# Optimization experiments

Measured on AMD Instinct MI355X. Metric: run time of the kernel, lower is better.

Reference implementation:

```python
import jax, jax.numpy as jnp
import numpy as np

B, N, C, H, REG = 1, 2309, 1024, 16, 5
D = C // H


def setup_inputs() -> dict:
    key = jax.random.key(0)
    k0, k1, k2, k3 = jax.random.split(key, 4)
    x = jax.random.normal(k0, (B, N, C), dtype=jnp.float32)
    g_info = jax.random.normal(k1, (12, 2, C), dtype=jnp.float32)
    W_qkv = jax.random.normal(k2, (C, 3 * C), dtype=jnp.float32) * 0.02
    W_proj = jax.random.normal(k3, (C, C), dtype=jnp.float32) * 0.02
    b_proj = jnp.zeros((C,), dtype=jnp.float32)
    return {"x": x, "g_info": g_info, "W_qkv": W_qkv, "W_proj": W_proj, "b_proj": b_proj}


def reference(x, g_info, W_qkv, W_proj, b_proj):
    Bx, Nx, Cx = x.shape
    scale = D ** -0.5
    # qkv projection (qkv_bias=False)
    qkv = (x @ W_qkv).reshape(Bx, Nx, 3, H, D)
    q, k, v = qkv[:, :, 0], qkv[:, :, 1], qkv[:, :, 2]  # [B,N,H,D]

    # grounding query vector from layer 0
    g_layer = g_info[0].reshape(-1, H, D)
    q_g = g_layer[0]  # [H,D]

    # cosine-similarity routing over non-register tokens
    q_pure = q[:, REG:]  # [B,M,H,D]
    q_n = q_pure / jnp.linalg.norm(q_pure, axis=-1, keepdims=True)
    qg_n = q_g / jnp.linalg.norm(q_g, axis=-1, keepdims=True)
    sim = (qg_n[None, None] * q_n).sum(-1).mean(-1)  # [B,M]
    sim = (sim - sim.min()) / (sim.max() - sim.min())  # global min-max normalize
    pos = sim > 0.9  # [B,M] boolean routing mask

    # Full logits computed once; group attention = masked softmax over the
    # group's key set (registers always included). This is mathematically
    # identical to the torch gather->attend->scatter, with static shapes.
    logits = jnp.einsum('bqhd,bkhd->bhqk', q * scale, k)  # [B,H,N,N]

    def masked_attn(tok_mask):
        key_mask = jnp.concatenate([jnp.ones((Bx, REG), bool), tok_mask], axis=1)  # [B,N]
        l = jnp.where(key_mask[:, None, None, :], logits, -jnp.inf)
        a = jax.nn.softmax(l, axis=-1)
        return jnp.einsum('bhqk,bkhd->bqhd', a, v)  # [B,N,H,D]

    x_pos = masked_attn(pos)
    x_neg = masked_attn(~pos)

    reg_out = (x_pos[:, :REG] + x_neg[:, :REG]) * 0.5
    tok_out = jnp.where(pos[:, :, None, None], x_pos[:, REG:], x_neg[:, REG:])
    out = jnp.concatenate([reg_out, tok_out], axis=1).reshape(Bx, Nx, Cx)
    return out @ W_proj + b_proj
```

## Files before the change

kernel.cpp:

```cpp
#include <hip/hip_runtime.h>
#include <math.h>

#define TOK 2309
#define CH 1024
#define NH 16
#define HD 64
#define NREG 5
#define NTOK (TOK - NREG)
#define NPADQ 2432
#define NPAD2 2432
#define NKT 38
#define HTILES 19
#define NQROW 2368
#define QSCL 0.1803368801f

typedef unsigned short ushort_t;
typedef unsigned char uchar_t;
typedef __attribute__((ext_vector_type(8))) short s8frag;
typedef __attribute__((ext_vector_type(4))) float f4frag;
typedef __attribute__((ext_vector_type(2))) long ll2;

__device__ __forceinline__ unsigned short f2bf(float x){
  union { float f; unsigned u; } v; v.f = x;
  unsigned r = v.u + 0x7FFF + ((v.u >> 16) & 1);
  return (unsigned short)(r >> 16);
}
__device__ __forceinline__ float bf2f(unsigned short u){
  union { unsigned u32; float f; } v; v.u32 = ((unsigned)u) << 16;
  return v.f;
}
__device__ __forceinline__ unsigned pack_bf16(float lo, float hi){
  union { float f; unsigned u; } a, b;
  a.f = lo; b.f = hi;
  return __builtin_amdgcn_perm(b.u + 0x8000u, a.u + 0x8000u, 0x07060302u);
}
__device__ __forceinline__ uchar_t f2fp8(float x){
  return (uchar_t)(__builtin_amdgcn_cvt_pk_fp8_f32(x, x, 0, false) & 0xff);
}
__device__ __forceinline__ void cp16(const void* g, void* l){
  __builtin_amdgcn_global_load_lds(
      (const __attribute__((address_space(1))) unsigned int*)g,
      (__attribute__((address_space(3))) unsigned int*)l, 16, 0, 0);
}

__global__ __launch_bounds__(256) void prep_kernel(
    const float* __restrict__ X, const float* __restrict__ Wqkv,
    const float* __restrict__ Wproj, const float* __restrict__ G,
    ushort_t* __restrict__ Xbf, ushort_t* __restrict__ WqkvT,
    ushort_t* __restrict__ WprojT, float* __restrict__ UT)
{
  const int tid = threadIdx.x;
  int bx = blockIdx.x;
  if (bx < NPADQ) {
    const int row = bx;
    const int c4 = tid * 4;
    ushort4 h4 = {0,0,0,0};
    if (row < TOK) {
      float4 v = *(const float4*)&X[(size_t)row*CH + c4];
      h4.x = f2bf(v.x); h4.y = f2bf(v.y); h4.z = f2bf(v.z); h4.w = f2bf(v.w);
    }
    *(ushort4*)&Xbf[(size_t)row*CH + c4] = h4;
    return;
  }
  bx -= NPADQ;
  if (bx < 1024) {
    __shared__ float T[64][68];
    int nb_i = bx & 63;
    const int k0 = (bx >> 6) * 64;
    const float* W; ushort_t* WT; int N;
    if (nb_i < 48) { W = Wqkv; WT = WqkvT; N = 3*CH; }
    else           { W = Wproj; WT = WprojT; N = CH; nb_i -= 48; }
    const int n0 = nb_i * 64;
    const int lr = tid >> 4;
    const int lc = (tid & 15) * 4;
    #pragma unroll
    for (int s = 0; s < 4; s++) {
      float4 v = *(const float4*)&W[(size_t)(k0 + lr + s*16) * N + n0 + lc];
      *(float4*)&T[lr + s*16][lc] = v;
    }
    __syncthreads();
    const int nl = tid >> 2;
    const int kc = (tid & 3) * 16;
    ushort_t* dh = WT + (size_t)(n0 + nl) * CH + k0 + kc;
    #pragma unroll
    for (int g = 0; g < 4; g++) {
      ushort4 oh;
      oh.x = f2bf(T[kc+g*4+0][nl]); oh.y = f2bf(T[kc+g*4+1][nl]);
      oh.z = f2bf(T[kc+g*4+2][nl]); oh.w = f2bf(T[kc+g*4+3][nl]);
      *(ushort4*)&dh[g*4] = oh;
    }
    return;
  }
  bx -= 1024;
  {
    const int k = bx * 16 + (tid >> 4);
    const int h = tid & 15;
    const float* g = G + h*64;
    float n2 = 0.f;
    #pragma unroll
    for (int d = 0; d < 64; d += 4) {
      float4 gv = *(const float4*)&g[d];
      n2 += gv.x*gv.x + gv.y*gv.y + gv.z*gv.z + gv.w*gv.w;
    }
    const float inv = 1.f / sqrtf(n2);
    const float* wr = Wqkv + (size_t)k*(3*CH) + h*64;
    float dot = 0.f;
    #pragma unroll
    for (int d = 0; d < 64; d += 4) {
      float4 wv = *(const float4*)&wr[d];
      float4 gv = *(const float4*)&g[d];
      dot += wv.x*gv.x + wv.y*gv.y + wv.z*gv.z + wv.w*gv.w;
    }
    UT[k*16 + h] = dot * inv;
  }
}

__global__ __launch_bounds__(256) void gemm_qkv_mfma(
    const ushort_t* __restrict__ Xbf, const ushort_t* __restrict__ WT,
    ushort_t* __restrict__ Qbf, uchar_t* __restrict__ Q8,
    uchar_t* __restrict__ K8, ushort_t* __restrict__ Vbf)
{
  __shared__ ushort_t LA[2][4096];
  __shared__ ushort_t LB[2][4096];
  const int tid = threadIdx.x;
  const int w = tid >> 6, lane = tid & 63;
  const int quad = lane >> 4, c16 = lane & 15;
  const int wm = w >> 1, wn = w & 1;
  const int nt = blockIdx.x, mt = blockIdx.y;
  const int n0 = nt * 128, m0 = mt * 128;

  const int srow = tid >> 2;
  const int g = (tid & 3) ^ ((tid >> 3) & 3);
  const size_t aoff = (size_t)(m0 + srow)*CH + g*8;
  const size_t boff = (size_t)(n0 + srow)*CH + g*8;
  const int lbase = (tid & 192) * 8;

  f4frag acc[4][4];
  #pragma unroll
  for (int mi = 0; mi < 4; mi++)
    #pragma unroll
    for (int nb = 0; nb < 4; nb++) acc[mi][nb] = (f4frag){0.f,0.f,0.f,0.f};

  const int soff = (quad ^ ((c16 >> 1) & 3)) * 8;
  int aro[4], bro[4];
  #pragma unroll
  for (int i = 0; i < 4; i++) {
    aro[i] = (wm*64 + i*16 + c16)*32 + soff;
    bro[i] = (wn*64 + i*16 + c16)*32 + soff;
  }

#define QKV_STAGE(KT, BUF) {                                                   \
    const int _k = (KT)*32;                                                    \
    cp16(Xbf + aoff + _k,                 &LA[BUF][lbase]);                    \
    cp16(Xbf + aoff + _k + (size_t)64*CH, &LA[BUF][2048 + lbase]);             \
    cp16(WT  + boff + _k,                 &LB[BUF][lbase]);                    \
    cp16(WT  + boff + _k + (size_t)64*CH, &LB[BUF][2048 + lbase]);             \
    }

  QKV_STAGE(0, 0);
  for (int kt = 0; kt < 32; kt++) {
    const int buf = kt & 1;
    __syncthreads();
    if (kt < 31) { QKV_STAGE(kt+1, buf^1); }
    s8frag a[4], b[4];
    #pragma unroll
    for (int i = 0; i < 4; i++) a[i] = *(const s8frag*)&LA[buf][aro[i]];
    #pragma unroll
    for (int i = 0; i < 4; i++) b[i] = *(const s8frag*)&LB[buf][bro[i]];
    #pragma unroll
    for (int mi = 0; mi < 4; mi++)
      #pragma unroll
      for (int nb = 0; nb < 4; nb++)
        acc[mi][nb] = __builtin_amdgcn_mfma_f32_16x16x32_bf16(a[mi], b[nb], acc[mi][nb], 0, 0, 0);
  }
#undef QKV_STAGE

  const int three = (nt >= 16) ? 2 : (nt >= 8) ? 1 : 0;
  #pragma unroll
  for (int mi = 0; mi < 4; mi++) {
    const int orow = m0 + wm*64 + mi*16 + quad*4;
    if (three == 0) {
      #pragma unroll
      for (int nb = 0; nb < 4; nb++) {
        const int col = n0 + wn*64 + nb*16 + c16;
        const int h = (col >> 6) & 15, d = col & 63;
        ushort_t* qb = Qbf + (size_t)h*NPADQ*64;
        uchar_t*  q8 = Q8 + (size_t)h*NPADQ*64;
        #pragma unroll
        for (int r = 0; r < 4; r++) {
          int row = orow + r;
          float v = (row < TOK) ? acc[mi][nb][r] : 0.f;
          qb[(size_t)row*64 + d] = f2bf(v);
          q8[(size_t)row*64 + d] = f2fp8(v);
        }
      }
    } else if (three == 1) {
      #pragma unroll
      for (int nb = 0; nb < 4; nb++) {
        const int col = n0 + wn*64 + nb*16 + c16;
        const int h = (col >> 6) & 15;
        const int quadK = ((nb & 1) * 2) + (c16 >> 3);
        const int byteoff = (nb >> 1) * 8 + (c16 & 7);
        uchar_t* base = K8 + (size_t)h*NKT*4096;
        #pragma unroll
        for (int r = 0; r < 4; r++) {
          int row = orow + r;
          float v = (row < TOK) ? acc[mi][nb][r] * QSCL : 0.f;
          int tile = row >> 6, b = (row >> 4) & 3, c16K = row & 15;
          base[(size_t)tile*4096 + b*1024 + (quadK*16 + c16K)*16 + byteoff] = f2fp8(v);
        }
      }
    } else {
      const int tile  = orow >> 6;
      const int jj    = orow & 63;
      const int c     = jj >> 5;
      const int t16   = (jj >> 4) & 1;
      const int quadA = (jj >> 2) & 3;
      #pragma unroll
      for (int nb = 0; nb < 4; nb++) {
        const int col = n0 + wn*64 + nb*16 + c16;
        const int h = (col >> 6) & 15, d = col & 63;
        const int dblk = d >> 4, c16A = d & 15;
        ushort_t* base = Vbf + (size_t)h*NKT*4096;
        ushort4 o;
        o.x = f2bf((orow+0 < TOK) ? acc[mi][nb][0] : 0.f);
        o.y = f2bf((orow+1 < TOK) ? acc[mi][nb][1] : 0.f);
        o.z = f2bf((orow+2 < TOK) ? acc[mi][nb][2] : 0.f);
        o.w = f2bf((orow+3 < TOK) ? acc[mi][nb][3] : 0.f);
        *(ushort4*)&base[(size_t)tile*4096 + dblk*1024 + c*512
                         + (quadA*16 + c16A)*8 + 4*t16] = o;
      }
    }
  }
}

__global__ __launch_bounds__(256) void sim_kernel(
    const float* __restrict__ X, const float* __restrict__ UT,
    const ushort_t* __restrict__ Qbf, float* __restrict__ sim)
{
  __shared__ float xs[1024];
  __shared__ float pnum[16][17];
  __shared__ float pn2[16][17];
  const int tid = threadIdx.x;
  const int row = NREG + blockIdx.x;
  *(float4*)&xs[tid*4] = *(const float4*)&X[(size_t)row*CH + tid*4];
  __syncthreads();
  const int h = tid & 15, seg = tid >> 4;
  const int k0 = seg * 64;
  float num = 0.f;
  #pragma unroll
  for (int j = 0; j < 64; j++)
    num += xs[k0 + j] * UT[(k0 + j)*16 + h];
  const ushort_t* qr = Qbf + ((size_t)h*NPADQ + row)*64 + seg*4;
  ushort4 a = *(const ushort4*)qr;
  float q0 = bf2f(a.x), q1 = bf2f(a.y), q2 = bf2f(a.z), q3 = bf2f(a.w);
  pnum[seg][h] = num;
  pn2[seg][h] = q0*q0 + q1*q1 + q2*q2 + q3*q3;
  __syncthreads();
  if (tid < 16) {
    float nsum = 0.f, dsum = 0.f;
    #pragma unroll
    for (int s = 0; s < 16; s++) { nsum += pnum[s][tid]; dsum += pn2[s][tid]; }
    float acc = nsum / sqrtf(dsum);
    acc += __shfl_xor(acc, 1, 64);
    acc += __shfl_xor(acc, 2, 64);
    acc += __shfl_xor(acc, 4, 64);
    acc += __shfl_xor(acc, 8, 64);
    if (tid == 0) sim[blockIdx.x] = acc * (1.0f/16.0f);
  }
}

__global__ __launch_bounds__(256) void mask_kernel(
    const float* __restrict__ sim, int* __restrict__ cls,
    float* __restrict__ WP, float* __restrict__ WN)
{
  __shared__ float smn[256], smx[256];
  const int tid = threadIdx.x;
  float mn = 1e30f, mx = -1e30f;
  for (int i = tid; i < NTOK; i += 256) { float s = sim[i]; mn = fminf(mn, s); mx = fmaxf(mx, s); }
  smn[tid] = mn; smx[tid] = mx;
  __syncthreads();
  for (int off = 128; off > 0; off >>= 1) {
    if (tid < off) { smn[tid] = fminf(smn[tid], smn[tid+off]); smx[tid] = fmaxf(smx[tid], smx[tid+off]); }
    __syncthreads();
  }
  mn = smn[0]; mx = smx[0];
  float inv = 1.0f / (mx - mn);
  for (int j = tid; j < NPAD2; j += 256) {
    float wp = 0.f, wn = 0.f; int c = 0;
    if (j < NREG) { wp = 1.f; wn = 1.f; c = 2; }
    else if (j < TOK) {
      bool pos = ((sim[j-NREG] - mn) * inv) > 0.9f;
      c = pos ? 1 : 0;
      wp = pos ? 1.f : 0.f;
      wn = pos ? 0.f : 1.f;
    }
    WP[j] = wp; WN[j] = wn;
    if (j < TOK) cls[j] = c;
  }
}

__global__ __launch_bounds__(256) void attn_kernel(
    const uchar_t* __restrict__ Q8, const uchar_t* __restrict__ K8,
    const ushort_t* __restrict__ Vbf,
    const float* __restrict__ WP, const float* __restrict__ WN,
    ushort_t* __restrict__ POp, ushort_t* __restrict__ POn,
    float* __restrict__ Lp, float* __restrict__ Ln)
{
  __shared__ __align__(16) uchar_t smem[24576];
  uchar_t* Kst = smem;
  uchar_t* Vst = smem + 8192;
  const int tid = threadIdx.x;
  const int w = tid >> 6, lane = tid & 63;
  const int quad = lane >> 4, c16 = lane & 15;
  const int h = blockIdx.y;
  const int half = blockIdx.z;
  const int q0 = blockIdx.x * 64;

  const uchar_t* Qh = Q8 + (size_t)h * NPADQ * 64;
  const uchar_t* gk = K8 + ((size_t)h*NKT + half*HTILES)*4096 + tid*16;
  const uchar_t* gv = (const uchar_t*)Vbf + ((size_t)h*NKT + half*HTILES)*8192 + tid*16;
  const int lw = w * 1024;

  const uchar_t* qp = Qh + (size_t)(q0 + w*16 + c16)*64 + quad*8;
  const long qf0 = *(const long*)(qp);
  const long qf1 = *(const long*)(qp + 32);

  f4frag op[4], on[4];
  #pragma unroll
  for (int nb = 0; nb < 4; nb++) { op[nb] = (f4frag){0.f,0.f,0.f,0.f}; on[nb] = (f4frag){0.f,0.f,0.f,0.f}; }
  float lp = 0.f, ln = 0.f;

  cp16(gk, Kst + lw);
  cp16(gv, Vst + lw);
  cp16(gv + 4096, Vst + 4096 + lw);

  int pb = 0;
  for (int t = 0; t < HTILES; t++) {
    __syncthreads();
    if (t < HTILES-1) {
      cp16(gk + (size_t)(t+1)*4096, Kst + (pb^1)*4096 + lw);
      cp16(gv + (size_t)(t+1)*8192,        Vst + (pb^1)*8192 + lw);
      cp16(gv + (size_t)(t+1)*8192 + 4096, Vst + (pb^1)*8192 + 4096 + lw);
    }
    const int j0 = half*(HTILES*64) + t*64;
    f4frag st[4];
    #pragma unroll
    for (int b = 0; b < 4; b++) {
      ll2 kv = *(const ll2*)&Kst[pb*4096 + b*1024 + lane*16];
      f4frag z = (f4frag){0.f,0.f,0.f,0.f};
      z     = __builtin_amdgcn_mfma_f32_16x16x32_fp8_fp8(kv.x, qf0, z, 0, 0, 0);
      st[b] = __builtin_amdgcn_mfma_f32_16x16x32_fp8_fp8(kv.y, qf1, z, 0, 0, 0);
    }
    unsigned pu[4][2], nu[4][2];
    #pragma unroll
    for (int b = 0; b < 4; b++) {
      float4 wp4 = *(const float4*)&WP[j0 + b*16 + quad*4];
      float4 wn4 = *(const float4*)&WN[j0 + b*16 + quad*4];
      float p0 = __builtin_amdgcn_exp2f(st[b][0]);
      float p1 = __builtin_amdgcn_exp2f(st[b][1]);
      float p2 = __builtin_amdgcn_exp2f(st[b][2]);
      float p3 = __builtin_amdgcn_exp2f(st[b][3]);
      float a0 = p0*wp4.x, a1 = p1*wp4.y, a2 = p2*wp4.z, a3 = p3*wp4.w;
      float b0 = p0*wn4.x, b1 = p1*wn4.y, b2 = p2*wn4.z, b3 = p3*wn4.w;
      lp += (a0+a1)+(a2+a3);
      ln += (b0+b1)+(b2+b3);
      pu[b][0] = pack_bf16(a0, a1); pu[b][1] = pack_bf16(a2, a3);
      nu[b][0] = pack_bf16(b0, b1); nu[b][1] = pack_bf16(b2, b3);
    }
    union Frag { unsigned u[4]; s8frag v; };
    Frag fp0, fp1, fn0, fn1;
    fp0.u[0]=pu[0][0]; fp0.u[1]=pu[0][1]; fp0.u[2]=pu[1][0]; fp0.u[3]=pu[1][1];
    fp1.u[0]=pu[2][0]; fp1.u[1]=pu[2][1]; fp1.u[2]=pu[3][0]; fp1.u[3]=pu[3][1];
    fn0.u[0]=nu[0][0]; fn0.u[1]=nu[0][1]; fn0.u[2]=nu[1][0]; fn0.u[3]=nu[1][1];
    fn1.u[0]=nu[2][0]; fn1.u[1]=nu[2][1]; fn1.u[2]=nu[3][0]; fn1.u[3]=nu[3][1];
    #pragma unroll
    for (int nb = 0; nb < 4; nb++) {
      s8frag va = *(const s8frag*)&Vst[pb*8192 + nb*2048 + lane*16];
      s8frag vb = *(const s8frag*)&Vst[pb*8192 + nb*2048 + 1024 + lane*16];
      op[nb] = __builtin_amdgcn_mfma_f32_16x16x32_bf16(va, fp0.v, op[nb], 0, 0, 0);
      op[nb] = __builtin_amdgcn_mfma_f32_16x16x32_bf16(vb, fp1.v, op[nb], 0, 0, 0);
      on[nb] = __builtin_amdgcn_mfma_f32_16x16x32_bf16(va, fn0.v, on[nb], 0, 0, 0);
      on[nb] = __builtin_amdgcn_mfma_f32_16x16x32_bf16(vb, fn1.v, on[nb], 0, 0, 0);
    }
    pb ^= 1;
  }

  lp += __shfl_xor(lp, 16, 64); lp += __shfl_xor(lp, 32, 64);
  ln += __shfl_xor(ln, 16, 64); ln += __shfl_xor(ln, 32, 64);
  const int iq = q0 + w*16 + c16;
  if (quad == 0 && iq < TOK) {
    Lp[((size_t)half*NH + h)*NQROW + iq] = lp;
    Ln[((size_t)half*NH + h)*NQROW + iq] = ln;
  }
  if (iq < TOK) {
    const size_t base = (size_t)half*NQROW*CH + (size_t)iq*CH + h*HD;
    #pragma unroll
    for (int nb = 0; nb < 4; nb++) {
      uint2 po, no;
      po.x = pack_bf16(op[nb][0], op[nb][1]);
      po.y = pack_bf16(op[nb][2], op[nb][3]);
      no.x = pack_bf16(on[nb][0], on[nb][1]);
      no.y = pack_bf16(on[nb][2], on[nb][3]);
      *(uint2*)(POp + base + nb*16 + quad*4) = po;
      *(uint2*)(POn + base + nb*16 + quad*4) = no;
    }
  }
}

__global__ __launch_bounds__(256) void merge_kernel(
    const ushort_t* __restrict__ POp, const ushort_t* __restrict__ POn,
    const float* __restrict__ Lp, const float* __restrict__ Ln,
    const int* __restrict__ cls, ushort_t* __restrict__ AObf)
{
  const int row = blockIdx.x;
  const int c4 = threadIdx.x * 4;
  const int h = c4 >> 6;
  const size_t o0 = (size_t)row*CH + c4;
  const size_t o1 = (size_t)NQROW*CH + o0;
  ushort4 p0 = *(const ushort4*)(POp + o0);
  ushort4 p1 = *(const ushort4*)(POp + o1);
  ushort4 n0 = *(const ushort4*)(POn + o0);
  ushort4 n1 = *(const ushort4*)(POn + o1);
  const float lpt = Lp[(size_t)h*NQROW + row] + Lp[(size_t)(NH+h)*NQROW + row];
  const float lnt = Ln[(size_t)h*NQROW + row] + Ln[(size_t)(NH+h)*NQROW + row];
  const float ilp = 1.f / lpt, iln = 1.f / lnt;
  const int cq = cls[row];
  float vp[4], vn[4], o[4];
  vp[0] = (bf2f(p0.x)+bf2f(p1.x))*ilp; vn[0] = (bf2f(n0.x)+bf2f(n1.x))*iln;
  vp[1] = (bf2f(p0.y)+bf2f(p1.y))*ilp; vn[1] = (bf2f(n0.y)+bf2f(n1.y))*iln;
  vp[2] = (bf2f(p0.z)+bf2f(p1.z))*ilp; vn[2] = (bf2f(n0.z)+bf2f(n1.z))*iln;
  vp[3] = (bf2f(p0.w)+bf2f(p1.w))*ilp; vn[3] = (bf2f(n0.w)+bf2f(n1.w))*iln;
  if (row < NREG) {
    #pragma unroll
    for (int i = 0; i < 4; i++) o[i] = 0.5f*(vp[i]+vn[i]);
  } else if (cq == 1) {
    #pragma unroll
    for (int i = 0; i < 4; i++) o[i] = vp[i];
  } else {
    #pragma unroll
    for (int i = 0; i < 4; i++) o[i] = vn[i];
  }
  uint2 pk;
  pk.x = pack_bf16(o[0], o[1]);
  pk.y = pack_bf16(o[2], o[3]);
  *(uint2*)(AObf + (size_t)row*CH + c4) = pk;
}

__global__ __launch_bounds__(256) void gemm_proj_mfma(
    const ushort_t* __restrict__ A, const ushort_t* __restrict__ WT,
    const float* __restrict__ bp, float* __restrict__ out)
{
  __shared__ ushort_t LA[2][4096];
  __shared__ ushort_t LB[2][2048];
  const int tid = threadIdx.x;
  const int w = tid >> 6, lane = tid & 63;
  const int quad = lane >> 4, c16 = lane & 15;
  const int wm = w >> 1, wn = w & 1;
  const int nt = blockIdx.x, mt = blockIdx.y;
  const int n0 = nt * 64, m0 = mt * 128;

  const int srow = tid >> 2;
  const int g = (tid & 3) ^ ((tid >> 3) & 3);
  const size_t aoff = (size_t)(m0 + srow)*CH + g*8;
  const size_t boff = (size_t)(n0 + srow)*CH + g*8;
  const int lbase = (tid & 192) * 8;

  f4frag acc[4][2];
  #pragma unroll
  for (int mi = 0; mi < 4; mi++)
    #pragma unroll
    for (int nb = 0; nb < 2; nb++) acc[mi][nb] = (f4frag){0.f,0.f,0.f,0.f};

  const int soff = (quad ^ ((c16 >> 1) & 3)) * 8;
  int aro[4], bro[2];
  #pragma unroll
  for (int i = 0; i < 4; i++) aro[i] = (wm*64 + i*16 + c16)*32 + soff;
  #pragma unroll
  for (int i = 0; i < 2; i++) bro[i] = (wn*32 + i*16 + c16)*32 + soff;

#define PROJ_STAGE(KT, BUF) {                                                  \
    const int _k = (KT)*32;                                                    \
    cp16(A  + aoff + _k,                 &LA[BUF][lbase]);                     \
    cp16(A  + aoff + _k + (size_t)64*CH, &LA[BUF][2048 + lbase]);              \
    cp16(WT + boff + _k,                 &LB[BUF][lbase]);                     \
    }

  PROJ_STAGE(0, 0);
  for (int kt = 0; kt < 32; kt++) {
    const int buf = kt & 1;
    __syncthreads();
    if (kt < 31) { PROJ_STAGE(kt+1, buf^1); }
    s8frag a[4], b[2];
    #pragma unroll
    for (int i = 0; i < 4; i++) a[i] = *(const s8frag*)&LA[buf][aro[i]];
    #pragma unroll
    for (int i = 0; i < 2; i++) b[i] = *(const s8frag*)&LB[buf][bro[i]];
    #pragma unroll
    for (int mi = 0; mi < 4; mi++)
      #pragma unroll
      for (int nb = 0; nb < 2; nb++)
        acc[mi][nb] = __builtin_amdgcn_mfma_f32_16x16x32_bf16(a[mi], b[nb], acc[mi][nb], 0, 0, 0);
  }
#undef PROJ_STAGE

  #pragma unroll
  for (int mi = 0; mi < 4; mi++) {
    const int orow = m0 + wm*64 + mi*16 + quad*4;
    #pragma unroll
    for (int nb = 0; nb < 2; nb++) {
      const int col = n0 + wn*32 + nb*16 + c16;
      const float bias = bp[col];
      #pragma unroll
      for (int r = 0; r < 4; r++) {
        int row = orow + r;
        if (row < TOK) out[(size_t)row*CH + col] = acc[mi][nb][r] + bias;
      }
    }
  }
}

extern "C" void kernel_launch(void* const* d_in, const int* in_sizes, int n_in,
                              void* d_out, int out_size, void* d_ws, size_t ws_size,
                              hipStream_t stream) {
  const float* x      = (const float*)d_in[0];
  const float* g_info = (const float*)d_in[1];
  const float* W_qkv  = (const float*)d_in[2];
  const float* W_proj = (const float*)d_in[3];
  const float* b_proj = (const float*)d_in[4];
  float* out = (float*)d_out;

  float* ws = (float*)d_ws;
  float* SIM = ws;
  float* WP  = SIM + NTOK;
  float* WN  = WP + NPAD2;
  int*   CLS = (int*)(WN + NPAD2);
  float* LpB = (float*)(CLS + 2312);
  float* LnB = LpB + (size_t)2*NH*NQROW;
  float* UT  = LnB + (size_t)2*NH*NQROW;
  ushort_t* Xbf    = (ushort_t*)(UT + (size_t)CH*NH);
  ushort_t* WqkvT  = Xbf    + (size_t)NPADQ*CH;
  ushort_t* WprojT = WqkvT  + (size_t)3*CH*CH;
  ushort_t* Qbf    = WprojT + (size_t)CH*CH;
  ushort_t* AObf   = Qbf    + (size_t)NH*NPADQ*64;
  ushort_t* POp    = AObf   + (size_t)NPADQ*CH;
  ushort_t* POn    = POp    + (size_t)2*NQROW*CH;
  uchar_t*  Q8     = (uchar_t*)(POn + (size_t)2*NQROW*CH);
  uchar_t*  K8     = Q8 + (size_t)NH*NPADQ*64;
  ushort_t* Vbf    = (ushort_t*)(K8 + (size_t)NH*NKT*4096);

  prep_kernel<<<dim3(NPADQ + 1024 + 64), 256, 0, stream>>>(
      x, W_qkv, W_proj, g_info, Xbf, WqkvT, WprojT, UT);
  gemm_qkv_mfma<<<dim3(24, 19), 256, 0, stream>>>(Xbf, WqkvT, Qbf, Q8, K8, Vbf);
  sim_kernel<<<dim3(NTOK), 256, 0, stream>>>(x, UT, Qbf, SIM);
  mask_kernel<<<dim3(1), 256, 0, stream>>>(SIM, CLS, WP, WN);
  attn_kernel<<<dim3(37, NH, 2), 256, 0, stream>>>(Q8, K8, Vbf, WP, WN,
                                                   POp, POn, LpB, LnB);
  merge_kernel<<<dim3(TOK), 256, 0, stream>>>(POp, POn, LpB, LnB, CLS, AObf);
  gemm_proj_mfma<<<dim3(16, 19), 256, 0, stream>>>(AObf, WprojT, b_proj, out);
}
```

Before: 232.2 us.

## Compute only each query's own group attention, dual path for registers only

Each non-register query row now computes only the masked attention for its own group (selected per lane via the class array), instead of both positive and negative groups. Only the first query block, which holds the register tokens, still computes both and writes fp32 partials to a small side buffer. This halves the PV MFMAs, exp masking work and partial-output traffic, and simplifies the merge kernel. The per-lane selection of the weight row and the divergent branch on the first block add small overhead.

Measured after the change: 240.2 us. 3.5% more time.

```diff
diff --git a/kernel.cpp b/kernel.cpp
--- a/kernel.cpp
+++ b/kernel.cpp
@@ -271,8 +271,7 @@
 }
 
 __global__ __launch_bounds__(256) void mask_kernel(
-    const float* __restrict__ sim, int* __restrict__ cls,
-    float* __restrict__ WP, float* __restrict__ WN)
+    const float* __restrict__ sim, int* __restrict__ cls, float* __restrict__ WSL)
 {
   __shared__ float smn[256], smx[256];
   const int tid = threadIdx.x;
@@ -295,7 +294,8 @@
       wp = pos ? 1.f : 0.f;
       wn = pos ? 0.f : 1.f;
     }
-    WP[j] = wp; WN[j] = wn;
+    WSL[j] = wn;
+    WSL[NPAD2 + j] = wp;
     if (j < TOK) cls[j] = c;
   }
 }
@@ -303,9 +303,10 @@
 __global__ __launch_bounds__(256) void attn_kernel(
     const uchar_t* __restrict__ Q8, const uchar_t* __restrict__ K8,
     const ushort_t* __restrict__ Vbf,
-    const float* __restrict__ WP, const float* __restrict__ WN,
-    ushort_t* __restrict__ POp, ushort_t* __restrict__ POn,
-    float* __restrict__ Lp, float* __restrict__ Ln)
+    const float* __restrict__ WSL, const int* __restrict__ cls,
+    ushort_t* __restrict__ POs, float* __restrict__ Ls,
+    float* __restrict__ Rp, float* __restrict__ Rn,
+    float* __restrict__ RLp, float* __restrict__ RLn)
 {
   __shared__ __align__(16) uchar_t smem[24576];
   uchar_t* Kst = smem;
@@ -316,6 +317,13 @@
   const int h = blockIdx.y;
   const int half = blockIdx.z;
   const int q0 = blockIdx.x * 64;
+  const bool dual = (blockIdx.x == 0);
+
+  const int iq = q0 + w*16 + c16;
+  const int cq = (iq < TOK) ? cls[iq] : 0;
+  const int sel = (cq != 0) ? 1 : 0;
+  const float* wsel = WSL + (size_t)sel*NPAD2;
+  const float* woth = WSL + (size_t)(1-sel)*NPAD2;
 
   const uchar_t* Qh = Q8 + (size_t)h * NPADQ * 64;
   const uchar_t* gk = K8 + ((size_t)h*NKT + half*HTILES)*4096 + tid*16;
@@ -335,6 +343,7 @@
   cp16(gv, Vst + lw);
   cp16(gv + 4096, Vst + 4096 + lw);
 
+  union Frag { unsigned u[4]; s8frag v; };
   int pb = 0;
   for (int t = 0; t < HTILES; t++) {
     __syncthreads();
@@ -355,91 +364,101 @@
     unsigned pu[4][2], nu[4][2];
     #pragma unroll
     for (int b = 0; b < 4; b++) {
-      float4 wp4 = *(const float4*)&WP[j0 + b*16 + quad*4];
-      float4 wn4 = *(const float4*)&WN[j0 + b*16 + quad*4];
+      float4 w4 = *(const float4*)&wsel[j0 + b*16 + quad*4];
       float p0 = __builtin_amdgcn_exp2f(st[b][0]);
       float p1 = __builtin_amdgcn_exp2f(st[b][1]);
       float p2 = __builtin_amdgcn_exp2f(st[b][2]);
       float p3 = __builtin_amdgcn_exp2f(st[b][3]);
-      float a0 = p0*wp4.x, a1 = p1*wp4.y, a2 = p2*wp4.z, a3 = p3*wp4.w;
-      float b0 = p0*wn4.x, b1 = p1*wn4.y, b2 = p2*wn4.z, b3 = p3*wn4.w;
+      float a0 = p0*w4.x, a1 = p1*w4.y, a2 = p2*w4.z, a3 = p3*w4.w;
       lp += (a0+a1)+(a2+a3);
-      ln += (b0+b1)+(b2+b3);
       pu[b][0] = pack_bf16(a0, a1); pu[b][1] = pack_bf16(a2, a3);
-      nu[b][0] = pack_bf16(b0, b1); nu[b][1] = pack_bf16(b2, b3);
-    }
-    union Frag { unsigned u[4]; s8frag v; };
-    Frag fp0, fp1, fn0, fn1;
+      if (dual) {
+        float4 wo = *(const float4*)&woth[j0 + b*16 + quad*4];
+        float b0 = p0*wo.x, b1 = p1*wo.y, b2 = p2*wo.z, b3 = p3*wo.w;
+        ln += (b0+b1)+(b2+b3);
+        nu[b][0] = pack_bf16(b0, b1); nu[b][1] = pack_bf16(b2, b3);
+      }
+    }
+    Frag fp0, fp1;
     fp0.u[0]=pu[0][0]; fp0.u[1]=pu[0][1]; fp0.u[2]=pu[1][0]; fp0.u[3]=pu[1][1];
     fp1.u[0]=pu[2][0]; fp1.u[1]=pu[2][1]; fp1.u[2]=pu[3][0]; fp1.u[3]=pu[3][1];
-    fn0.u[0]=nu[0][0]; fn0.u[1]=nu[0][1]; fn0.u[2]=nu[1][0]; fn0.u[3]=nu[1][1];
-    fn1.u[0]=nu[2][0]; fn1.u[1]=nu[2][1]; fn1.u[2]=nu[3][0]; fn1.u[3]=nu[3][1];
+    Frag fn0, fn1;
+    if (dual) {
+      fn0.u[0]=nu[0][0]; fn0.u[1]=nu[0][1]; fn0.u[2]=nu[1][0]; fn0.u[3]=nu[1][1];
+      fn1.u[0]=nu[2][0]; fn1.u[1]=nu[2][1]; fn1.u[2]=nu[3][0]; fn1.u[3]=nu[3][1];
+    }
     #pragma unroll
     for (int nb = 0; nb < 4; nb++) {
       s8frag va = *(const s8frag*)&Vst[pb*8192 + nb*2048 + lane*16];
       s8frag vb = *(const s8frag*)&Vst[pb*8192 + nb*2048 + 1024 + lane*16];
       op[nb] = __builtin_amdgcn_mfma_f32_16x16x32_bf16(va, fp0.v, op[nb], 0, 0, 0);
       op[nb] = __builtin_amdgcn_mfma_f32_16x16x32_bf16(vb, fp1.v, op[nb], 0, 0, 0);
-      on[nb] = __builtin_amdgcn_mfma_f32_16x16x32_bf16(va, fn0.v, on[nb], 0, 0, 0);
-      on[nb] = __builtin_amdgcn_mfma_f32_16x16x32_bf16(vb, fn1.v, on[nb], 0, 0, 0);
+      if (dual) {
+        on[nb] = __builtin_amdgcn_mfma_f32_16x16x32_bf16(va, fn0.v, on[nb], 0, 0, 0);
+        on[nb] = __builtin_amdgcn_mfma_f32_16x16x32_bf16(vb, fn1.v, on[nb], 0, 0, 0);
+      }
     }
     pb ^= 1;
   }
 
   lp += __shfl_xor(lp, 16, 64); lp += __shfl_xor(lp, 32, 64);
-  ln += __shfl_xor(ln, 16, 64); ln += __shfl_xor(ln, 32, 64);
-  const int iq = q0 + w*16 + c16;
-  if (quad == 0 && iq < TOK) {
-    Lp[((size_t)half*NH + h)*NQROW + iq] = lp;
-    Ln[((size_t)half*NH + h)*NQROW + iq] = ln;
-  }
+  if (quad == 0 && iq < TOK) Ls[((size_t)half*NH + h)*NQROW + iq] = lp;
   if (iq < TOK) {
     const size_t base = (size_t)half*NQROW*CH + (size_t)iq*CH + h*HD;
     #pragma unroll
     for (int nb = 0; nb < 4; nb++) {
-      uint2 po, no;
+      uint2 po;
       po.x = pack_bf16(op[nb][0], op[nb][1]);
       po.y = pack_bf16(op[nb][2], op[nb][3]);
-      no.x = pack_bf16(on[nb][0], on[nb][1]);
-      no.y = pack_bf16(on[nb][2], on[nb][3]);
-      *(uint2*)(POp + base + nb*16 + quad*4) = po;
-      *(uint2*)(POn + base + nb*16 + quad*4) = no;
+      *(uint2*)(POs + base + nb*16 + quad*4) = po;
+    }
+  }
+  if (dual && w == 0 && c16 < NREG) {
+    ln += __shfl_xor(ln, 16, 64); ln += __shfl_xor(ln, 32, 64);
+    float* rp = Rp + (((size_t)half*NH + h)*NREG + c16)*64;
+    float* rn = Rn + (((size_t)half*NH + h)*NREG + c16)*64;
+    #pragma unroll
+    for (int nb = 0; nb < 4; nb++) {
+      *(f4frag*)&rp[nb*16 + quad*4] = op[nb];
+      *(f4frag*)&rn[nb*16 + quad*4] = on[nb];
+    }
+    if (quad == 0) {
+      RLp[((size_t)half*NH + h)*NREG + c16] = lp;
+      RLn[((size_t)half*NH + h)*NREG + c16] = ln;
     }
   }
 }
 
 __global__ __launch_bounds__(256) void merge_kernel(
-    const ushort_t* __restrict__ POp, const ushort_t* __restrict__ POn,
-    const float* __restrict__ Lp, const float* __restrict__ Ln,
-    const int* __restrict__ cls, ushort_t* __restrict__ AObf)
+    const ushort_t* __restrict__ POs, const float* __restrict__ Ls,
+    const float* __restrict__ Rp, const float* __restrict__ Rn,
+    const float* __restrict__ RLp, const float* __restrict__ RLn,
+    ushort_t* __restrict__ AObf)
 {
   const int row = blockIdx.x;
   const int c4 = threadIdx.x * 4;
   const int h = c4 >> 6;
-  const size_t o0 = (size_t)row*CH + c4;
-  const size_t o1 = (size_t)NQROW*CH + o0;
-  ushort4 p0 = *(const ushort4*)(POp + o0);
-  ushort4 p1 = *(const ushort4*)(POp + o1);
-  ushort4 n0 = *(const ushort4*)(POn + o0);
-  ushort4 n1 = *(const ushort4*)(POn + o1);
-  const float lpt = Lp[(size_t)h*NQROW + row] + Lp[(size_t)(NH+h)*NQROW + row];
-  const float lnt = Ln[(size_t)h*NQROW + row] + Ln[(size_t)(NH+h)*NQROW + row];
-  const float ilp = 1.f / lpt, iln = 1.f / lnt;
-  const int cq = cls[row];
-  float vp[4], vn[4], o[4];
-  vp[0] = (bf2f(p0.x)+bf2f(p1.x))*ilp; vn[0] = (bf2f(n0.x)+bf2f(n1.x))*iln;
-  vp[1] = (bf2f(p0.y)+bf2f(p1.y))*ilp; vn[1] = (bf2f(n0.y)+bf2f(n1.y))*iln;
-  vp[2] = (bf2f(p0.z)+bf2f(p1.z))*ilp; vn[2] = (bf2f(n0.z)+bf2f(n1.z))*iln;
-  vp[3] = (bf2f(p0.w)+bf2f(p1.w))*ilp; vn[3] = (bf2f(n0.w)+bf2f(n1.w))*iln;
-  if (row < NREG) {
-    #pragma unroll
-    for (int i = 0; i < 4; i++) o[i] = 0.5f*(vp[i]+vn[i]);
-  } else if (cq == 1) {
-    #pragma unroll
-    for (int i = 0; i < 4; i++) o[i] = vp[i];
+  float o[4];
+  if (row >= NREG) {
+    const size_t o0 = (size_t)row*CH + c4;
+    ushort4 p0 = *(const ushort4*)(POs + o0);
+    ushort4 p1 = *(const ushort4*)(POs + (size_t)NQROW*CH + o0);
+    const float lt = Ls[(size_t)h*NQROW + row] + Ls[(size_t)(NH+h)*NQROW + row];
+    const float il = 1.f / lt;
+    o[0] = (bf2f(p0.x)+bf2f(p1.x))*il;
+    o[1] = (bf2f(p0.y)+bf2f(p1.y))*il;
+    o[2] = (bf2f(p0.z)+bf2f(p1.z))*il;
+    o[3] = (bf2f(p0.w)+bf2f(p1.w))*il;
   } else {
-    #pragma unroll
-    for (int i = 0; i < 4; i++) o[i] = vn[i];
+    const int d = c4 & 63;
+    const size_t i0 = ((size_t)h*NREG + row)*64 + d;
+    const size_t i1 = ((size_t)(NH+h)*NREG + row)*64 + d;
+    const float lpt = RLp[(size_t)h*NREG + row] + RLp[(size_t)(NH+h)*NREG + row];
+    const float lnt = RLn[(size_t)h*NREG + row] + RLn[(size_t)(NH+h)*NREG + row];
+    const float ilp = 0.5f / lpt, iln = 0.5f / lnt;
+    #pragma unroll
+    for (int i = 0; i < 4; i++)
+      o[i] = (Rp[i0+i] + Rp[i1+i])*ilp + (Rn[i0+i] + Rn[i1+i])*iln;
   }
   uint2 pk;
   pk.x = pack_bf16(o[0], o[1]);
@@ -532,20 +551,21 @@
 
   float* ws = (float*)d_ws;
   float* SIM = ws;
-  float* WP  = SIM + NTOK;
-  float* WN  = WP + NPAD2;
-  int*   CLS = (int*)(WN + NPAD2);
-  float* LpB = (float*)(CLS + 2312);
-  float* LnB = LpB + (size_t)2*NH*NQROW;
-  float* UT  = LnB + (size_t)2*NH*NQROW;
-  ushort_t* Xbf    = (ushort_t*)(UT + (size_t)CH*NH);
+  float* WSL = SIM + NTOK;
+  int*   CLS = (int*)(WSL + 2*NPAD2);
+  float* LsB = (float*)(CLS + 2312);
+  float* UT  = LsB + (size_t)2*NH*NQROW;
+  float* Rp  = UT + (size_t)CH*NH;
+  float* Rn  = Rp + (size_t)2*NH*NREG*64;
+  float* RLp = Rn + (size_t)2*NH*NREG*64;
+  float* RLn = RLp + (size_t)2*NH*NREG;
+  ushort_t* Xbf    = (ushort_t*)(RLn + (size_t)2*NH*NREG);
   ushort_t* WqkvT  = Xbf    + (size_t)NPADQ*CH;
   ushort_t* WprojT = WqkvT  + (size_t)3*CH*CH;
   ushort_t* Qbf    = WprojT + (size_t)CH*CH;
   ushort_t* AObf   = Qbf    + (size_t)NH*NPADQ*64;
-  ushort_t* POp    = AObf   + (size_t)NPADQ*CH;
-  ushort_t* POn    = POp    + (size_t)2*NQROW*CH;
-  uchar_t*  Q8     = (uchar_t*)(POn + (size_t)2*NQROW*CH);
+  ushort_t* POs    = AObf   + (size_t)NPADQ*CH;
+  uchar_t*  Q8     = (uchar_t*)(POs + (size_t)2*NQROW*CH);
   uchar_t*  K8     = Q8 + (size_t)NH*NPADQ*64;
   ushort_t* Vbf    = (ushort_t*)(K8 + (size_t)NH*NKT*4096);
 
@@ -553,9 +573,9 @@
       x, W_qkv, W_proj, g_info, Xbf, WqkvT, WprojT, UT);
   gemm_qkv_mfma<<<dim3(24, 19), 256, 0, stream>>>(Xbf, WqkvT, Qbf, Q8, K8, Vbf);
   sim_kernel<<<dim3(NTOK), 256, 0, stream>>>(x, UT, Qbf, SIM);
-  mask_kernel<<<dim3(1), 256, 0, stream>>>(SIM, CLS, WP, WN);
-  attn_kernel<<<dim3(37, NH, 2), 256, 0, stream>>>(Q8, K8, Vbf, WP, WN,
-                                                   POp, POn, LpB, LnB);
-  merge_kernel<<<dim3(TOK), 256, 0, stream>>>(POp, POn, LpB, LnB, CLS, AObf);
+  mask_kernel<<<dim3(1), 256, 0, stream>>>(SIM, CLS, WSL);
+  attn_kernel<<<dim3(37, NH, 2), 256, 0, stream>>>(Q8, K8, Vbf, WSL, CLS,
+                                                   POs, LsB, Rp, Rn, RLp, RLn);
+  merge_kernel<<<dim3(TOK), 256, 0, stream>>>(POs, LsB, Rp, Rn, RLp, RLn, AObf);
   gemm_proj_mfma<<<dim3(16, 19), 256, 0, stream>>>(AObf, WprojT, b_proj, out);
 }
```
